# Kernel tuning notes

Hardware: AMD Instinct MI355X
Metric: run time of the kernel (lower is better)

The kernel has to match this reference:

```python
import jax, jax.numpy as jnp
import numpy as np

D = 4096          # in_features == out_features (scale broadcast requires square W)
TOKENS = 16384


def setup_inputs() -> dict:
    key = jax.random.key(0)
    kx, kq, ks, kb = jax.random.split(key, 4)
    x = jax.random.normal(kx, (TOKENS, D), dtype=jnp.float32)
    # int4 quantized weights in [-8, 7] (stored int8 in torch; int32 here is fine)
    qweight = jax.random.randint(kq, (D, D), -8, 8, dtype=jnp.int32)
    # per-channel scales: positive, realistic magnitude ~ max|W|/7
    scale = jax.random.uniform(ks, (D,), dtype=jnp.float32, minval=1e-3, maxval=2e-2)
    bias = jax.random.normal(kb, (D,), dtype=jnp.float32)
    return {"x": x, "qweight": qweight, "scale": scale, "bias": bias}


def reference(x, qweight, scale, bias):
    # Dequantize: W[i, j] = qW[i, j] * scale[i]  (scale.view(-1,1) in the source)
    W = qweight.astype(jnp.float32) * scale[:, None]   # [out, in]
    # F.linear(x, W, bias) = x @ W.T + bias
    return x @ W.T + bias                               # [tokens, out]
```

## Files before the change

kernel.cpp:

```cpp
#include <hip/hip_runtime.h>

typedef __attribute__((ext_vector_type(4))) int  i8x16;
typedef __attribute__((ext_vector_type(4))) int  i32x4;
typedef __attribute__((ext_vector_type(8))) short bf16x8;
typedef __attribute__((ext_vector_type(8))) unsigned short ushort8;
typedef __attribute__((ext_vector_type(4))) float f32x4;

__device__ __forceinline__ unsigned short f32_to_bf16(float f) {
    union { float f; unsigned int u; } v;
    v.f = f;
    unsigned int r = v.u + (0x7fffu + ((v.u >> 16) & 1u));
    return (unsigned short)(r >> 16);
}

__device__ __forceinline__ void gload_lds16(const void* g, void* l) {
    __builtin_amdgcn_global_load_lds(
        (const __attribute__((address_space(1))) unsigned int*)g,
        (__attribute__((address_space(3))) unsigned int*)l, 16, 0, 0);
}

__global__ __launch_bounds__(256) void quantx_kernel(const float* __restrict__ x,
                                                     char* __restrict__ xq,
                                                     float* __restrict__ rs, int K) {
    const int row = blockIdx.x;
    const float4* xr = (const float4*)(x + (size_t)row * K);
    const int K4 = K >> 2;
    const int t = threadIdx.x;
    float am = 0.f;
    for (int i = t; i < K4; i += 256) {
        float4 v = xr[i];
        am = fmaxf(am, fmaxf(fmaxf(fabsf(v.x), fabsf(v.y)),
                             fmaxf(fabsf(v.z), fabsf(v.w))));
    }
    for (int off = 32; off; off >>= 1) am = fmaxf(am, __shfl_xor(am, off));
    __shared__ float ws[4];
    if ((t & 63) == 0) ws[t >> 6] = am;
    __syncthreads();
    am = fmaxf(fmaxf(ws[0], ws[1]), fmaxf(ws[2], ws[3]));
    const float inv = am > 0.f ? 127.f / am : 0.f;
    if (t == 0) rs[row] = am > 0.f ? am / 127.f : 0.f;
    int* dst = (int*)(xq + (size_t)row * K);
    for (int i = t; i < K4; i += 256) {
        float4 v = xr[i];
        int a = (int)rintf(v.x * inv), b = (int)rintf(v.y * inv);
        int c = (int)rintf(v.z * inv), d = (int)rintf(v.w * inv);
        dst[i] = (a & 255) | ((b & 255) << 8) | ((c & 255) << 16) | (d << 24);
    }
}

__global__ void convq_kernel(const int* __restrict__ q, char* __restrict__ qb, long n16) {
    long i = (long)blockIdx.x * blockDim.x + threadIdx.x;
    const long stride = (long)gridDim.x * blockDim.x;
    for (; i < n16; i += stride) {
        const int4* p = (const int4*)(q + i * 16);
        int4 a = p[0], b = p[1], c = p[2], d = p[3];
        int4 r;
        r.x = (a.x & 255) | ((a.y & 255) << 8) | ((a.z & 255) << 16) | (a.w << 24);
        r.y = (b.x & 255) | ((b.y & 255) << 8) | ((b.z & 255) << 16) | (b.w << 24);
        r.z = (c.x & 255) | ((c.y & 255) << 8) | ((c.z & 255) << 16) | (c.w << 24);
        r.w = (d.x & 255) | ((d.y & 255) << 8) | ((d.z & 255) << 16) | (d.w << 24);
        ((int4*)qb)[i] = r;
    }
}

__global__ __launch_bounds__(512, 2) void qgemm_i8_kernel(
    const char* __restrict__ A, const char* __restrict__ B,
    const float* __restrict__ rs, const float* __restrict__ scale,
    const float* __restrict__ bias, float* __restrict__ C, int M, int N, int K) {
    extern __shared__ char sm[];

    const int tid  = threadIdx.x;
    const int lane = tid & 63;
    const int w    = tid >> 6;
    const int wr   = w >> 2;
    const int wc   = w & 3;
    const int l15  = lane & 15;
    const int l4   = lane >> 4;
    const int r7   = l15 & 7;

    const int nwg = gridDim.x;
    const int bid = blockIdx.x;
    const int swz = (bid & 7) * (nwg >> 3) + (bid >> 3);
    const int nbx = N >> 8;
    const int m0  = (swz / nbx) << 8;
    const int n0  = (swz % nbx) << 8;

    const int c0 = tid, c1 = tid + 512;
    const size_t inv0 = (size_t)(c0 >> 3) * K + (size_t)((((c0 & 7) ^ ((c0 >> 3) & 7))) << 4);
    const size_t inv1 = (size_t)(c1 >> 3) * K + (size_t)((((c1 & 7) ^ ((c1 >> 3) & 7))) << 4);
    const int ldst0 = w << 10;
    const int ldst1 = (w << 10) + 8192;

#define STAGE(ldsHalf, gsrc) do {                         \
        gload_lds16((gsrc) + inv0, (ldsHalf) + ldst0);    \
        gload_lds16((gsrc) + inv1, (ldsHalf) + ldst1); } while (0)

    const int aRow0 = (wr * 128 + l15) * 128;
    const int bRow0 = (wc * 64 + l15) * 128;
    const int sl0   = ((0 + l4) ^ r7) << 4;
    const int sl1   = ((4 + l4) ^ r7) << 4;

    const char* pA = A + (size_t)m0 * K;
    const char* pB = B + (size_t)n0 * K;
    const size_t hK = (size_t)128 * K;
    const int NT = K >> 7;

    i32x4 acc[8][4];
#pragma unroll
    for (int m = 0; m < 8; ++m)
#pragma unroll
        for (int n = 0; n < 4; ++n) acc[m][n] = (i32x4){0, 0, 0, 0};

#define RD_A(DST, BUF, MB)                                                     \
    _Pragma("unroll") for (int m = 0; m < 4; ++m) {                            \
        (DST)[m][0] = *(const i8x16*)((BUF) + aRow0 + ((MB) + m) * 2048 + sl0); \
        (DST)[m][1] = *(const i8x16*)((BUF) + aRow0 + ((MB) + m) * 2048 + sl1); }
#define RD_B(DST, BUF, NB)                                                     \
    _Pragma("unroll") for (int n = 0; n < 2; ++n) {                            \
        (DST)[n][0] = *(const i8x16*)((BUF) + bRow0 + ((NB) + n) * 2048 + sl0); \
        (DST)[n][1] = *(const i8x16*)((BUF) + bRow0 + ((NB) + n) * 2048 + sl1); }
#define MFMA8(AF, BF, MB, NB)                                                  \
    _Pragma("unroll") for (int kk = 0; kk < 2; ++kk)                           \
    _Pragma("unroll") for (int m = 0; m < 4; ++m)                              \
    _Pragma("unroll") for (int n = 0; n < 2; ++n)                              \
        acc[(MB) + m][(NB) + n] = __builtin_amdgcn_mfma_i32_16x16x64_i8(       \
            (AF)[m][kk], (BF)[n][kk], acc[(MB) + m][(NB) + n], 0, 0, 0);
#define LGKM(N) do { asm volatile("s_waitcnt lgkmcnt(" #N ")" ::: "memory");   \
                     __builtin_amdgcn_sched_barrier(0); } while (0)

    i8x16 aF0[4][2], aF1[4][2], bF01[2][2], bF23[2][2];

    STAGE(sm + 0,      pA);
    STAGE(sm + 16384,  pA + hK);
    STAGE(sm + 65536,  pB);
    STAGE(sm + 81920,  pB + hK);
    if (NT > 1) {
        STAGE(sm + 98304,  pB + 128);
        STAGE(sm + 114688, pB + hK + 128);
        asm volatile("s_waitcnt vmcnt(4)" ::: "memory");
    } else {
        asm volatile("s_waitcnt vmcnt(0)" ::: "memory");
    }
    __builtin_amdgcn_s_barrier();
    __builtin_amdgcn_sched_barrier(0);
    RD_A(aF0, sm, 0);
    RD_B(bF01, sm + 65536, 0);
    RD_B(bF23, sm + 65536, 2);

    for (int t = 0; t < NT; ++t) {
        const int cur = t & 1;
        char* Ab = sm + cur * 32768;
        char* Bb = sm + 65536 + cur * 32768;
        char* An = sm + (cur ^ 1) * 32768;
        char* Bn = sm + 65536 + (cur ^ 1) * 32768;
        const int k1 = (t + 1) << 7;
        const int k2 = (t + 2) << 7;

        if (t + 1 < NT) {
            STAGE(An,         pA + k1);
            STAGE(An + 16384, pA + hK + k1);
        }
        LGKM(4);
        __builtin_amdgcn_s_setprio(1);
        MFMA8(aF0, bF01, 0, 0);
        __builtin_amdgcn_s_setprio(0);

        RD_A(aF1, Ab, 4);
        LGKM(8);
        __builtin_amdgcn_s_setprio(1);
        MFMA8(aF0, bF23, 0, 2);
        __builtin_amdgcn_s_setprio(0);
        asm volatile("s_waitcnt vmcnt(0)" ::: "memory");
        __builtin_amdgcn_s_barrier();

        if (t + 2 < NT) STAGE(Bb, pB + k2);
        LGKM(0);
        __builtin_amdgcn_s_setprio(1);
        MFMA8(aF1, bF01, 4, 0);
        __builtin_amdgcn_s_setprio(0);
        if (t + 1 < NT) {
            RD_A(aF0, An, 0);
            RD_B(bF01, Bn, 0);
        }

        if (t + 2 < NT) STAGE(Bb + 16384, pB + hK + k2);
        __builtin_amdgcn_s_setprio(1);
        MFMA8(aF1, bF23, 4, 2);
        __builtin_amdgcn_s_setprio(0);
        if (t + 1 < NT) RD_B(bF23, Bn, 2);
        __builtin_amdgcn_s_barrier();
    }

#pragma unroll
    for (int n = 0; n < 4; ++n) {
        const int col = n0 + wc * 64 + n * 16 + l15;
        const float sc = scale[col];
        const float bs = bias[col];
#pragma unroll
        for (int m = 0; m < 8; ++m) {
            const int row0 = m0 + wr * 128 + m * 16 + l4 * 4;
#pragma unroll
            for (int j = 0; j < 4; ++j)
                C[(size_t)(row0 + j) * N + col] =
                    (float)acc[m][n][j] * (rs[row0 + j] * sc) + bs;
        }
    }
#undef STAGE
#undef RD_A
#undef RD_B
#undef MFMA8
#undef LGKM
}

__global__ __launch_bounds__(256) void qgemm_fb_kernel(
    const float* __restrict__ Af, const int* __restrict__ Bi,
    const float* __restrict__ scale, const float* __restrict__ bias,
    float* __restrict__ C, int M, int N, int K) {
    constexpr int BK = 64;
    __shared__ unsigned short lA[128 * BK];
    __shared__ unsigned short lB[128 * BK];
    const int t = threadIdx.x, lane = t & 63, w = t >> 6;
    const int wr = w >> 1, wc = w & 1;
    const int m0 = blockIdx.y * 128, n0 = blockIdx.x * 128;
    const int l15 = lane & 15, l4 = lane >> 4;
    f32x4 acc[4][4];
#pragma unroll
    for (int m = 0; m < 4; ++m)
#pragma unroll
        for (int n = 0; n < 4; ++n) acc[m][n] = (f32x4){0.f, 0.f, 0.f, 0.f};
    for (int k0 = 0; k0 < K; k0 += BK) {
        __syncthreads();
#pragma unroll
        for (int i = 0; i < 4; ++i) {
            const int off = i * 4096 + w * 1024 + lane * 16;
            const int row = off >> 7;
            const int col = (off & 127) >> 1;
            const float* pa = Af + (size_t)(m0 + row) * K + k0 + col;
            float4 a0 = *(const float4*)pa;
            float4 a1 = *(const float4*)(pa + 4);
            ushort8 va;
            va[0] = f32_to_bf16(a0.x); va[1] = f32_to_bf16(a0.y);
            va[2] = f32_to_bf16(a0.z); va[3] = f32_to_bf16(a0.w);
            va[4] = f32_to_bf16(a1.x); va[5] = f32_to_bf16(a1.y);
            va[6] = f32_to_bf16(a1.z); va[7] = f32_to_bf16(a1.w);
            *(ushort8*)((char*)lA + off) = va;
            const int* pb = Bi + (size_t)(n0 + row) * K + k0 + col;
            int4 b0 = *(const int4*)pb;
            int4 b1 = *(const int4*)(pb + 4);
            ushort8 vb;
            vb[0] = f32_to_bf16((float)b0.x); vb[1] = f32_to_bf16((float)b0.y);
            vb[2] = f32_to_bf16((float)b0.z); vb[3] = f32_to_bf16((float)b0.w);
            vb[4] = f32_to_bf16((float)b1.x); vb[5] = f32_to_bf16((float)b1.y);
            vb[6] = f32_to_bf16((float)b1.z); vb[7] = f32_to_bf16((float)b1.w);
            *(ushort8*)((char*)lB + off) = vb;
        }
        __syncthreads();
#pragma unroll
        for (int kk = 0; kk < BK; kk += 32) {
            bf16x8 af[4], bfr[4];
#pragma unroll
            for (int m = 0; m < 4; ++m)
                af[m] = *(const bf16x8*)&lA[(wr * 64 + m * 16 + l15) * BK + kk + l4 * 8];
#pragma unroll
            for (int n = 0; n < 4; ++n)
                bfr[n] = *(const bf16x8*)&lB[(wc * 64 + n * 16 + l15) * BK + kk + l4 * 8];
#pragma unroll
            for (int m = 0; m < 4; ++m)
#pragma unroll
                for (int n = 0; n < 4; ++n)
                    acc[m][n] = __builtin_amdgcn_mfma_f32_16x16x32_bf16(
                        af[m], bfr[n], acc[m][n], 0, 0, 0);
        }
    }
#pragma unroll
    for (int n = 0; n < 4; ++n) {
        const int col = n0 + wc * 64 + n * 16 + l15;
        const float sc = scale[col], bs = bias[col];
#pragma unroll
        for (int m = 0; m < 4; ++m) {
            const int row0 = m0 + wr * 64 + m * 16 + l4 * 4;
#pragma unroll
            for (int j = 0; j < 4; ++j)
                C[(size_t)(row0 + j) * N + col] = fmaf(acc[m][n][j], sc, bs);
        }
    }
}

extern "C" void kernel_launch(void* const* d_in, const int* in_sizes, int n_in,
                              void* d_out, int out_size, void* d_ws, size_t ws_size,
                              hipStream_t stream) {
    const float* x     = (const float*)d_in[0];
    const int*   q     = (const int*)d_in[1];
    const float* scale = (const float*)d_in[2];
    const float* bias  = (const float*)d_in[3];
    float*       out   = (float*)d_out;

    const int K = in_sizes[2];
    const int N = in_sizes[1] / K;
    const int M = in_sizes[0] / K;

    const size_t xq_b = (size_t)M * K;
    const size_t qb_b = (size_t)N * K;
    const size_t need = xq_b + qb_b + (size_t)M * 4;
    const int nwg = (M / 256) * (N / 256);

    if (ws_size >= need && (M % 256) == 0 && (N % 256) == 0 &&
        (K % 128) == 0 && K >= 256 && (nwg % 8) == 0) {
        char*  xq = (char*)d_ws;
        char*  qb = xq + xq_b;
        float* rs = (float*)(qb + qb_b);
        quantx_kernel<<<M, 256, 0, stream>>>(x, xq, rs, K);
        convq_kernel<<<2048, 256, 0, stream>>>(q, qb, (long)(qb_b / 16));
        qgemm_i8_kernel<<<nwg, 512, 131072, stream>>>(xq, qb, rs, scale, bias,
                                                      out, M, N, K);
    } else {
        dim3 grid(N / 128, M / 128);
        qgemm_fb_kernel<<<grid, 256, 0, stream>>>(x, q, scale, bias, out, M, N, K);
    }
}
```

Baseline: 368.3 us.

## Load B fragments directly from global into registers, halve LDS usage

The B operand is no longer staged through LDS. Each lane loads its B fragments straight from global memory into registers, double-buffered across two register sets, while A keeps its LDS double buffer. Dynamic LDS drops from 128 KB to 64 KB, which may allow two workgroups per CU, and the loop is unrolled by two tiles. The cost is uncoalesced-ish 16-byte global reads of B repeated across waves without LDS sharing, more VGPR pressure, and simpler waitcnt scheduling that gives up the finer-grained interleaving.

```diff
diff --git a/kernel.cpp b/kernel.cpp
--- a/kernel.cpp
+++ b/kernel.cpp
@@ -91,104 +91,83 @@
     const int ldst0 = w << 10;
     const int ldst1 = (w << 10) + 8192;
 
-#define STAGE(ldsHalf, gsrc) do {                         \
-        gload_lds16((gsrc) + inv0, (ldsHalf) + ldst0);    \
-        gload_lds16((gsrc) + inv1, (ldsHalf) + ldst1); } while (0)
+#define STAGE_A(buf, gsrc) do {                           \
+        gload_lds16((gsrc) + inv0, (buf) + ldst0);        \
+        gload_lds16((gsrc) + inv1, (buf) + ldst1); } while (0)
 
     const int aRow0 = (wr * 128 + l15) * 128;
-    const int bRow0 = (wc * 64 + l15) * 128;
     const int sl0   = ((0 + l4) ^ r7) << 4;
     const int sl1   = ((4 + l4) ^ r7) << 4;
 
     const char* pA = A + (size_t)m0 * K;
-    const char* pB = B + (size_t)n0 * K;
     const size_t hK = (size_t)128 * K;
     const int NT = K >> 7;
 
+    const char* pBl = B + (size_t)(n0 + wc * 64 + l15) * K + (l4 << 4);
+    const size_t bStride = (size_t)K << 4;
+
     i32x4 acc[8][4];
 #pragma unroll
     for (int m = 0; m < 8; ++m)
 #pragma unroll
         for (int n = 0; n < 4; ++n) acc[m][n] = (i32x4){0, 0, 0, 0};
 
+#define LOADB(DST, T) do {                                                     \
+    _Pragma("unroll") for (int nf = 0; nf < 4; ++nf)                           \
+    _Pragma("unroll") for (int kk = 0; kk < 2; ++kk)                           \
+        (DST)[nf][kk] = *(const i8x16*)(pBl + (size_t)nf * bStride +           \
+                                        (size_t)(T) * 128 + kk * 64); } while (0)
 #define RD_A(DST, BUF, MB)                                                     \
     _Pragma("unroll") for (int m = 0; m < 4; ++m) {                            \
         (DST)[m][0] = *(const i8x16*)((BUF) + aRow0 + ((MB) + m) * 2048 + sl0); \
         (DST)[m][1] = *(const i8x16*)((BUF) + aRow0 + ((MB) + m) * 2048 + sl1); }
-#define RD_B(DST, BUF, NB)                                                     \
-    _Pragma("unroll") for (int n = 0; n < 2; ++n) {                            \
-        (DST)[n][0] = *(const i8x16*)((BUF) + bRow0 + ((NB) + n) * 2048 + sl0); \
-        (DST)[n][1] = *(const i8x16*)((BUF) + bRow0 + ((NB) + n) * 2048 + sl1); }
-#define MFMA8(AF, BF, MB, NB)                                                  \
+#define MFMA_H(AF, BC, MB)                                                     \
     _Pragma("unroll") for (int kk = 0; kk < 2; ++kk)                           \
     _Pragma("unroll") for (int m = 0; m < 4; ++m)                              \
-    _Pragma("unroll") for (int n = 0; n < 2; ++n)                              \
-        acc[(MB) + m][(NB) + n] = __builtin_amdgcn_mfma_i32_16x16x64_i8(       \
-            (AF)[m][kk], (BF)[n][kk], acc[(MB) + m][(NB) + n], 0, 0, 0);
-#define LGKM(N) do { asm volatile("s_waitcnt lgkmcnt(" #N ")" ::: "memory");   \
+    _Pragma("unroll") for (int nf = 0; nf < 4; ++nf)                           \
+        acc[(MB) + m][nf] = __builtin_amdgcn_mfma_i32_16x16x64_i8(             \
+            (AF)[m][kk], (BC)[nf][kk], acc[(MB) + m][nf], 0, 0, 0);
+#define LGKM0() do { asm volatile("s_waitcnt lgkmcnt(0)" ::: "memory");        \
                      __builtin_amdgcn_sched_barrier(0); } while (0)
 
-    i8x16 aF0[4][2], aF1[4][2], bF01[2][2], bF23[2][2];
-
-    STAGE(sm + 0,      pA);
-    STAGE(sm + 16384,  pA + hK);
-    STAGE(sm + 65536,  pB);
-    STAGE(sm + 81920,  pB + hK);
-    if (NT > 1) {
-        STAGE(sm + 98304,  pB + 128);
-        STAGE(sm + 114688, pB + hK + 128);
-        asm volatile("s_waitcnt vmcnt(4)" ::: "memory");
-    } else {
-        asm volatile("s_waitcnt vmcnt(0)" ::: "memory");
-    }
+    i8x16 aF0[4][2], aF1[4][2], bX[4][2], bY[4][2];
+
+    STAGE_A(sm,         pA);
+    STAGE_A(sm + 16384, pA + hK);
+    LOADB(bX, 0);
+    asm volatile("s_waitcnt vmcnt(8)" ::: "memory");
     __builtin_amdgcn_s_barrier();
-    __builtin_amdgcn_sched_barrier(0);
-    RD_A(aF0, sm, 0);
-    RD_B(bF01, sm + 65536, 0);
-    RD_B(bF23, sm + 65536, 2);
-
-    for (int t = 0; t < NT; ++t) {
-        const int cur = t & 1;
-        char* Ab = sm + cur * 32768;
-        char* Bb = sm + 65536 + cur * 32768;
-        char* An = sm + (cur ^ 1) * 32768;
-        char* Bn = sm + 65536 + (cur ^ 1) * 32768;
-        const int k1 = (t + 1) << 7;
-        const int k2 = (t + 2) << 7;
-
-        if (t + 1 < NT) {
-            STAGE(An,         pA + k1);
-            STAGE(An + 16384, pA + hK + k1);
-        }
-        LGKM(4);
-        __builtin_amdgcn_s_setprio(1);
-        MFMA8(aF0, bF01, 0, 0);
-        __builtin_amdgcn_s_setprio(0);
-
-        RD_A(aF1, Ab, 4);
-        LGKM(8);
-        __builtin_amdgcn_s_setprio(1);
-        MFMA8(aF0, bF23, 0, 2);
-        __builtin_amdgcn_s_setprio(0);
-        asm volatile("s_waitcnt vmcnt(0)" ::: "memory");
-        __builtin_amdgcn_s_barrier();
-
-        if (t + 2 < NT) STAGE(Bb, pB + k2);
-        LGKM(0);
-        __builtin_amdgcn_s_setprio(1);
-        MFMA8(aF1, bF01, 4, 0);
-        __builtin_amdgcn_s_setprio(0);
-        if (t + 1 < NT) {
-            RD_A(aF0, An, 0);
-            RD_B(bF01, Bn, 0);
-        }
-
-        if (t + 2 < NT) STAGE(Bb + 16384, pB + hK + k2);
-        __builtin_amdgcn_s_setprio(1);
-        MFMA8(aF1, bF23, 4, 2);
-        __builtin_amdgcn_s_setprio(0);
-        if (t + 1 < NT) RD_B(bF23, Bn, 2);
-        __builtin_amdgcn_s_barrier();
+
+#define TILE(T, AB, AN, BCUR, BNXT) do {                                       \
+        const int k1_ = ((T) + 1) << 7;                                        \
+        if ((T) + 1 < NT) {                                                    \
+            STAGE_A((AN),         pA + k1_);                \
+            STAGE_A((AN) + 16384, pA + hK + k1_);                              \
+            LOADB(BNXT, (T) + 1);                           \
+        }                                                                      \
+        RD_A(aF0, (AB), 0);                                                    \
+        LGKM0();                                                               \
+        __builtin_amdgcn_s_setprio(1);                                         \
+        MFMA_H(aF0, BCUR, 0);                                                  \
+        __builtin_amdgcn_s_setprio(0);                                         \
+        RD_A(aF1, (AB), 4);                                                    \
+        LGKM0();                                                               \
+        __builtin_amdgcn_s_setprio(1);                                         \
+        MFMA_H(aF1, BCUR, 4);                                                  \
+        __builtin_amdgcn_s_setprio(0);                                         \
+        if ((T) + 1 < NT) asm volatile("s_waitcnt vmcnt(8)" ::: "memory");     \
+        else              asm volatile("s_waitcnt vmcnt(0)" ::: "memory");     \
+        __builtin_amdgcn_s_barrier();      \
+    } while (0)
+
+    for (int t = 0; t < NT; t += 2) {
+        char* Ab = sm + (t & 2 ? 32768 : 0);
+        char* cur = sm + ((t & 1) ? 32768 : 0);
+        (void)Ab; (void)cur;
+        char* b0 = sm + ((t & 1) * 32768);
+        char* b1 = sm + (((t + 1) & 1) * 32768);
+        TILE(t,     b0, b1, bX, bY);
+        TILE(t + 1, b1, b0, bY, bX);
     }
 
 #pragma unroll
@@ -205,11 +184,12 @@
                     (float)acc[m][n][j] * (rs[row0 + j] * sc) + bs;
         }
     }
-#undef STAGE
+#undef STAGE_A
+#undef LOADB
 #undef RD_A
-#undef RD_B
-#undef MFMA8
-#undef LGKM
+#undef MFMA_H
+#undef LGKM0
+#undef TILE
 }
 
 __global__ __launch_bounds__(256) void qgemm_fb_kernel(
@@ -305,14 +285,14 @@
     const int nwg = (M / 256) * (N / 256);
 
     if (ws_size >= need && (M % 256) == 0 && (N % 256) == 0 &&
-        (K % 128) == 0 && K >= 256 && (nwg % 8) == 0) {
+        (K % 256) == 0 && (nwg % 8) == 0) {
         char*  xq = (char*)d_ws;
         char*  qb = xq + xq_b;
         float* rs = (float*)(qb + qb_b);
         quantx_kernel<<<M, 256, 0, stream>>>(x, xq, rs, K);
         convq_kernel<<<2048, 256, 0, stream>>>(q, qb, (long)(qb_b / 16));
-        qgemm_i8_kernel<<<nwg, 512, 131072, stream>>>(xq, qb, rs, scale, bias,
-                                                      out, M, N, K);
+        qgemm_i8_kernel<<<nwg, 512, 65536, stream>>>(xq, qb, rs, scale, bias,
+                                                     out, M, N, K);
     } else {
         dim3 grid(N / 128, M / 128);
         qgemm_fb_kernel<<<grid, 256, 0, stream>>>(x, q, scale, bias, out, M, N, K);
```

New measurement: 621.6 us. +68.8%, slower.
